# Optimization experiments

Measured on AMD Instinct MI355X. Metric: run time of the kernel, lower is better.

The kernel has to match this reference:

```python
import jax, jax.numpy as jnp
import numpy as np

B = 16384   # batch
S = 6       # fixed number of ABR frequencies
H = 8       # num_heads
HD = 64     # head_dim
D = H * HD  # model width = head_dim * num_heads


def _pe(d):
    # FrequencyPositionalEncoding: pe[i, 0::2] = sin(f_i * div), pe[i, 1::2] = cos(f_i * div)
    freqs = np.array([6.0, 12.0, 18.0, 24.0, 30.0, 0.0], np.float32) / 30.0
    div = np.exp(np.arange(0, d, 2, dtype=np.float32) * (-np.log(10000.0) / d))
    pe = np.zeros((S, d), np.float32)
    pe[:, 0::2] = np.sin(freqs[:, None] * div)
    pe[:, 1::2] = np.cos(freqs[:, None] * div)
    return jnp.asarray(pe)


def _freq_bias():
    # adjacent-frequency bias 0.1, octave pairs (0,1),(1,3) overwritten to 0.05
    b = np.zeros((S, S), np.float32)
    for i in range(S - 1):
        b[i, i + 1] = 0.1
        b[i + 1, i] = 0.1
    for i, j in [(0, 1), (1, 3)]:
        b[i, j] = 0.05
        b[j, i] = 0.05
    return jnp.asarray(b)


def setup_inputs() -> dict:
    key = jax.random.key(0)
    ks = jax.random.split(key, 6)

    def w(k, shape, s=0.05):
        return jax.random.normal(k, shape, jnp.float32) * s

    return {
        "x": jax.random.normal(ks[0], (B, S), jnp.float32),
        "W_in": w(ks[1], (1, D)), "b_in": jnp.zeros((D,), jnp.float32),
        "Wq": w(ks[2], (D, D)), "bq": jnp.zeros((D,), jnp.float32),
        "Wk": w(ks[3], (D, D)), "bk": jnp.zeros((D,), jnp.float32),
        "Wv": w(ks[4], (D, D)), "bv": jnp.zeros((D,), jnp.float32),
        "Wo": w(ks[5], (D, 1)), "bo": jnp.zeros((1,), jnp.float32),
        "gamma": jnp.ones((D,), jnp.float32),
        "beta": jnp.zeros((D,), jnp.float32),
    }


def reference(x, W_in, b_in, Wq, bq, Wk, bk, Wv, bv, Wo, bo, gamma, beta):
    Bn, Sn = x.shape
    Dn = gamma.shape[0]
    hd = Dn // H
    # input projection: scalar token -> D   (Linear(1, D))
    tok = x[..., None] * W_in[0] + b_in                      # (B, S, D)
    tok = tok + _pe(Dn)[None]                                # frequency positional encoding
    # LayerNorm (eps=1e-5)
    mu = tok.mean(-1, keepdims=True)
    var = tok.var(-1, keepdims=True)
    tok = (tok - mu) * jax.lax.rsqrt(var + 1e-5) * gamma + beta
    # q/k/v projections, split heads
    q = (tok @ Wq + bq).reshape(Bn, Sn, H, hd)
    k = (tok @ Wk + bk).reshape(Bn, Sn, H, hd)
    v = (tok @ Wv + bv).reshape(Bn, Sn, H, hd)
    scores = jnp.einsum('bihd,bjhd->bhij', q, k) * (hd ** -0.5)
    scores = scores + _freq_bias()[None, None]               # (B, H, S, S)
    attn = jax.nn.softmax(scores, axis=-1)                   # dropout = identity (eval)
    attended = jnp.einsum('bhij,bjhd->bihd', attn, v).reshape(Bn, Sn, Dn)
    out = (attended @ Wo + bo)[..., 0] + x                   # (B, S) residual
    return out, attn.mean(axis=1)
```

## Files before the change

kernel.cpp:

```cpp
#include <hip/hip_runtime.h>
#include <math.h>

#define WS_STATS 0
#define WS_T     16

__constant__ float FREQ_BIAS[36] = {
    0.0f, 0.05f, 0.0f, 0.0f, 0.0f, 0.0f,
    0.05f, 0.0f, 0.1f, 0.05f, 0.0f, 0.0f,
    0.0f, 0.1f, 0.0f, 0.1f, 0.0f, 0.0f,
    0.0f, 0.05f, 0.1f, 0.0f, 0.1f, 0.0f,
    0.0f, 0.0f, 0.0f, 0.1f, 0.0f, 0.1f,
    0.0f, 0.0f, 0.0f, 0.0f, 0.1f, 0.0f
};

__global__ __launch_bounds__(256) void kA(
    const float* __restrict__ W_in, const float* __restrict__ b_in,
    const float* __restrict__ gamma, const float* __restrict__ beta,
    const float* __restrict__ Wq, const float* __restrict__ bq,
    const float* __restrict__ Wk, const float* __restrict__ bk,
    const float* __restrict__ Wv, const float* __restrict__ bv,
    float* __restrict__ ws, float* __restrict__ part)
{
    __shared__ float ls[8][512];
    __shared__ float partial[4][8][64];
    __shared__ float red[13][4];

    const int tid = threadIdx.x, wave = tid >> 6, lane = tid & 63;
    const int bid = blockIdx.x;
    const int rc = bid & 7, cg = (bid >> 3) & 7, p = bid >> 6;

    const float k_ln = 0.0179889457300305367f;
    const float freqs[6] = {0.2f, 0.4f, 0.6f, 0.8f, 1.0f, 0.0f};
    float wd[2], cc2[2][6], gm[2], bt[2];
    #pragma unroll
    for (int q = 0; q < 2; ++q) {
        const int d = tid + q * 256;
        wd[q] = W_in[d];
        gm[q] = gamma[d];
        bt[q] = beta[d];
        float dv = __expf(-(float)(d & ~1) * k_ln);
        float bi = b_in[d];
        bool odd = (d & 1);
        #pragma unroll
        for (int s = 0; s < 6; ++s) {
            float ph = freqs[s] * dv;
            cc2[q][s] = bi + (odd ? __cosf(ph) : __sinf(ph));
        }
    }
    {
        float sums[7];
        sums[0] = wd[0] + wd[1];
        #pragma unroll
        for (int s = 0; s < 6; ++s) sums[1 + s] = cc2[0][s] + cc2[1][s];
        #pragma unroll
        for (int m = 1; m < 64; m <<= 1) {
            #pragma unroll
            for (int k = 0; k < 7; ++k) sums[k] += __shfl_xor(sums[k], m, 64);
        }
        if (lane == 0) {
            #pragma unroll
            for (int k = 0; k < 7; ++k) red[k][wave] = sums[k];
        }
    }
    __syncthreads();
    const float mw = (red[0][0] + red[0][1] + red[0][2] + red[0][3]) * (1.0f / 512.0f);
    float mc[6];
    #pragma unroll
    for (int s = 0; s < 6; ++s)
        mc[s] = (red[1 + s][0] + red[1 + s][1] + red[1 + s][2] + red[1 + s][3]) * (1.0f / 512.0f);
    __syncthreads();

    float hw[2], hc[2][6];
    #pragma unroll
    for (int q = 0; q < 2; ++q) {
        hw[q] = wd[q] - mw;
        #pragma unroll
        for (int s = 0; s < 6; ++s) hc[q][s] = cc2[q][s] - mc[s];
    }

    if (bid == 0) {
        float moms[13];
        moms[0] = hw[0] * hw[0] + hw[1] * hw[1];
        #pragma unroll
        for (int s = 0; s < 6; ++s) {
            moms[1 + s] = hw[0] * hc[0][s] + hw[1] * hc[1][s];
            moms[7 + s] = hc[0][s] * hc[0][s] + hc[1][s] * hc[1][s];
        }
        #pragma unroll
        for (int m = 1; m < 64; m <<= 1) {
            #pragma unroll
            for (int k = 0; k < 13; ++k) moms[k] += __shfl_xor(moms[k], m, 64);
        }
        if (lane == 0) {
            #pragma unroll
            for (int k = 0; k < 13; ++k) red[k][wave] = moms[k];
        }
    }
    #pragma unroll
    for (int q = 0; q < 2; ++q) {
        const int d = tid + q * 256;
        ls[0][d] = hw[q] * gm[q];
        #pragma unroll
        for (int s = 0; s < 6; ++s) ls[1 + s][d] = hc[q][s] * gm[q];
        ls[7][d] = bt[q];
    }
    __syncthreads();
    if (bid == 0 && tid < 13)
        ws[WS_STATS + tid] = (red[tid][0] + red[tid][1] + red[tid][2] + red[tid][3]) * (1.0f / 512.0f);

    const float* W  = (p == 0) ? Wq : ((p == 1) ? Wk : Wv);
    const float* bb = (p == 0) ? bq : ((p == 1) ? bk : bv);
    const int col = (cg << 6) | lane;
    const int row0 = (rc << 6) | (wave << 4);
    float acc[8] = {0.f, 0.f, 0.f, 0.f, 0.f, 0.f, 0.f, 0.f};
    #pragma unroll
    for (int rr = 0; rr < 16; ++rr) {
        const float wv = W[(row0 + rr) * 512 + col];
        #pragma unroll
        for (int v = 0; v < 8; ++v) acc[v] = fmaf(wv, ls[v][row0 + rr], acc[v]);
    }
    #pragma unroll
    for (int v = 0; v < 8; ++v) partial[wave][v][lane] = acc[v];
    __syncthreads();
    #pragma unroll
    for (int ii = 0; ii < 2; ++ii) {
        const int idx = tid + ii * 256;
        const int v = idx >> 6, cx = idx & 63;
        float t = partial[0][v][cx] + partial[1][v][cx]
                + partial[2][v][cx] + partial[3][v][cx];
        if (v == 7 && rc == 0) t += bb[(cg << 6) | cx];
        part[(size_t)bid * 512 + idx] = t;
    }
}

__global__ __launch_bounds__(256) void kB(const float* __restrict__ part,
                                          const float* __restrict__ Wo,
                                          float* __restrict__ ws)
{
    __shared__ float ab[24][65];
    const int tid = threadIdx.x;
    const int h = blockIdx.x;

    for (int e = tid; e < 24 * 64; e += 256) {
        const int vp = e >> 6, c = e & 63;
        const int p = vp >> 3, v = vp & 7;
        const int stripe = p * 8 + h;
        float t = 0.f;
        #pragma unroll
        for (int rcx = 0; rcx < 8; ++rcx)
            t += part[(size_t)(stripe * 8 + rcx) * 512 + v * 64 + c];
        ab[vp][c] = t;
    }
    __syncthreads();

    if (tid < 64) {
        const int a = tid >> 3, b2 = tid & 7;
        float acc = 0.f;
        #pragma unroll
        for (int c = 0; c < 64; ++c)
            acc = fmaf(ab[a][c], ab[8 + b2][c], acc);
        ws[WS_T + (h << 6) + tid] = acc * 0.125f;
    } else if (tid < 72) {
        const int a = tid - 64;
        float acc = 0.f;
        #pragma unroll
        for (int c = 0; c < 64; ++c)
            acc = fmaf(ab[16 + a][c], Wo[(h << 6) + c], acc);
        ws[WS_T + 512 + (h << 3) + a] = acc;
    }
}

__global__ __launch_bounds__(256) void kC(const float* __restrict__ x,
                                          const float* __restrict__ ws,
                                          const float* __restrict__ bo,
                                          float* __restrict__ out, int total)
{
    __shared__ float T_s[592];
    const int tid = threadIdx.x;
    for (int e = tid; e < 589; e += 256)
        T_s[e] = (e < 576) ? ws[WS_T + e] : ws[WS_STATS + (e - 576)];
    __syncthreads();

    const int g = blockIdx.x * 256 + tid;
    if (g >= total) return;
    const unsigned b = (unsigned)g / 6u;
    const int i = g - (int)b * 6;

    const float* D8 = T_s;
    const float* VD = T_s + 512;
    const float vw = T_s[576];
    const float* cov = T_s + 577;
    const float* vc = T_s + 583;
    const float bo0 = bo[0];

    const float2* xp = (const float2*)(x + (size_t)b * 6u);
    const float2 x01 = xp[0], x23 = xp[1], x45 = xp[2];
    const float al[6] = {x01.x, x01.y, x23.x, x23.y, x45.x, x45.y};

    float r[6], u[6];
    #pragma unroll
    for (int j = 0; j < 6; ++j) {
        float a = al[j];
        float var = fmaf(a, fmaf(a, vw, 2.0f * cov[j]), vc[j]) + 1e-5f;
        r[j] = rsqrtf(var);
        u[j] = a * r[j];
    }

    float bias[6];
    #pragma unroll
    for (int j = 0; j < 6; ++j) bias[j] = FREQ_BIAS[i * 6 + j];

    const float r_i = r[i], u_i = u[i];
    float acc = 0.f;
    float am[6] = {0.f, 0.f, 0.f, 0.f, 0.f, 0.f};

    #pragma unroll
    for (int h = 0; h < 8; ++h) {
        const float* Dh = D8 + h * 64;
        const float* Vh = VD + h * 8;
        const float P1 = Dh[0], P5 = Dh[7], P7 = Dh[56], P9 = Dh[63];
        const float P3i = Dh[(1 + i) * 8], P6i = Dh[(1 + i) * 8 + 7];

        float s[6];
        #pragma unroll
        for (int j = 0; j < 6; ++j) {
            float t1 = fmaf(u[j], P1, fmaf(r[j], Dh[1 + j], P5));
            float t2 = fmaf(u[j], P3i, fmaf(r[j], Dh[(1 + i) * 8 + 1 + j], P6i));
            float t3 = fmaf(u[j], P7, fmaf(r[j], Dh[57 + j], P9));
            s[j] = fmaf(u_i, t1, fmaf(r_i, t2, t3)) + bias[j];
        }
        float m = s[0];
        #pragma unroll
        for (int j = 1; j < 6; ++j) m = fmaxf(m, s[j]);
        float e[6], ssum = 0.f;
        #pragma unroll
        for (int j = 0; j < 6; ++j) { e[j] = __expf(s[j] - m); ssum += e[j]; }
        const float inv = 1.0f / ssum;

        const float av = Vh[0], cvv = Vh[7];
        float ha = 0.f;
        #pragma unroll
        for (int j = 0; j < 6; ++j) {
            float a = e[j] * inv;
            am[j] += a;
            float vp = fmaf(u[j], av, r[j] * Vh[1 + j]);
            ha = fmaf(a, vp, ha);
        }
        acc += ha + cvv;
    }

    out[g] = acc + bo0 + al[i];

    float2* amp = (float2*)(out + total + (size_t)g * 6u);
    amp[0] = make_float2(am[0] * 0.125f, am[1] * 0.125f);
    amp[1] = make_float2(am[2] * 0.125f, am[3] * 0.125f);
    amp[2] = make_float2(am[4] * 0.125f, am[5] * 0.125f);
}

extern "C" void kernel_launch(void* const* d_in, const int* in_sizes, int n_in,
                              void* d_out, int out_size, void* d_ws, size_t ws_size,
                              hipStream_t stream) {
    const float* x     = (const float*)d_in[0];
    const float* W_in  = (const float*)d_in[1];
    const float* b_in  = (const float*)d_in[2];
    const float* Wq    = (const float*)d_in[3];
    const float* bq    = (const float*)d_in[4];
    const float* Wk    = (const float*)d_in[5];
    const float* bk    = (const float*)d_in[6];
    const float* Wv    = (const float*)d_in[7];
    const float* bv    = (const float*)d_in[8];
    const float* Wo    = (const float*)d_in[9];
    const float* bo    = (const float*)d_in[10];
    const float* gamma = (const float*)d_in[11];
    const float* beta  = (const float*)d_in[12];
    float* ws  = (float*)d_ws;
    float* out = (float*)d_out;

    const int total = in_sizes[0];

    kA<<<192, 256, 0, stream>>>(W_in, b_in, gamma, beta, Wq, bq, Wk, bk, Wv, bv, ws, out);
    kB<<<8, 256, 0, stream>>>(out, Wo, ws);
    kC<<<(total + 255) / 256, 256, 0, stream>>>(x, ws, bo, out, total);
}
```

Measured before the change: 20.63 us.

## Split LayerNorm prep into its own kernel and widen projection and output blocks

```diff
diff --git a/kernel.cpp b/kernel.cpp
--- a/kernel.cpp
+++ b/kernel.cpp
@@ -3,6 +3,7 @@
 
 #define WS_STATS 0
 #define WS_T     16
+#define WS_LS    600
 
 __constant__ float FREQ_BIAS[36] = {
     0.0f, 0.05f, 0.0f, 0.0f, 0.0f, 0.0f,
@@ -13,123 +14,137 @@
     0.0f, 0.0f, 0.0f, 0.0f, 0.1f, 0.0f
 };
 
-__global__ __launch_bounds__(256) void kA(
-    const float* __restrict__ W_in, const float* __restrict__ b_in,
-    const float* __restrict__ gamma, const float* __restrict__ beta,
+__global__ __launch_bounds__(512) void kP(const float* __restrict__ W_in,
+                                          const float* __restrict__ b_in,
+                                          const float* __restrict__ gamma,
+                                          const float* __restrict__ beta,
+                                          float* __restrict__ ws)
+{
+    __shared__ float red[13][8];
+    const int d = threadIdx.x, wave = d >> 6, lane = d & 63;
+
+    const float k_ln = 0.0179889457300305367f;
+    const float freqs[6] = {0.2f, 0.4f, 0.6f, 0.8f, 1.0f, 0.0f};
+    const float wd = W_in[d];
+    const float gm = gamma[d];
+    const float bt = beta[d];
+    const float bi = b_in[d];
+    const float dv = __expf(-(float)(d & ~1) * k_ln);
+    const bool odd = (d & 1);
+    float c[6];
+    #pragma unroll
+    for (int s = 0; s < 6; ++s) {
+        float ph = freqs[s] * dv;
+        c[s] = bi + (odd ? __cosf(ph) : __sinf(ph));
+    }
+
+    float sums[7];
+    sums[0] = wd;
+    #pragma unroll
+    for (int s = 0; s < 6; ++s) sums[1 + s] = c[s];
+    #pragma unroll
+    for (int m = 1; m < 64; m <<= 1) {
+        #pragma unroll
+        for (int k = 0; k < 7; ++k) sums[k] += __shfl_xor(sums[k], m, 64);
+    }
+    if (lane == 0) {
+        #pragma unroll
+        for (int k = 0; k < 7; ++k) red[k][wave] = sums[k];
+    }
+    __syncthreads();
+    float mw = 0.f, mc[6] = {0.f, 0.f, 0.f, 0.f, 0.f, 0.f};
+    #pragma unroll
+    for (int j = 0; j < 8; ++j) mw += red[0][j];
+    mw *= (1.0f / 512.0f);
+    #pragma unroll
+    for (int s = 0; s < 6; ++s) {
+        float t = 0.f;
+        #pragma unroll
+        for (int j = 0; j < 8; ++j) t += red[1 + s][j];
+        mc[s] = t * (1.0f / 512.0f);
+    }
+    __syncthreads();
+
+    const float hw = wd - mw;
+    float hc[6];
+    #pragma unroll
+    for (int s = 0; s < 6; ++s) hc[s] = c[s] - mc[s];
+
+    float moms[13];
+    moms[0] = hw * hw;
+    #pragma unroll
+    for (int s = 0; s < 6; ++s) { moms[1 + s] = hw * hc[s]; moms[7 + s] = hc[s] * hc[s]; }
+    #pragma unroll
+    for (int m = 1; m < 64; m <<= 1) {
+        #pragma unroll
+        for (int k = 0; k < 13; ++k) moms[k] += __shfl_xor(moms[k], m, 64);
+    }
+    if (lane == 0) {
+        #pragma unroll
+        for (int k = 0; k < 13; ++k) red[k][wave] = moms[k];
+    }
+    __syncthreads();
+    if (d < 13) {
+        float t = 0.f;
+        #pragma unroll
+        for (int j = 0; j < 8; ++j) t += red[d][j];
+        ws[WS_STATS + d] = t * (1.0f / 512.0f);
+    }
+
+    float4 f0 = make_float4(hw * gm, hc[0] * gm, hc[1] * gm, hc[2] * gm);
+    float4 f1 = make_float4(hc[3] * gm, hc[4] * gm, hc[5] * gm, bt);
+    *(float4*)&ws[WS_LS + d * 8]     = f0;
+    *(float4*)&ws[WS_LS + d * 8 + 4] = f1;
+}
+
+__global__ __launch_bounds__(512) void kA(
     const float* __restrict__ Wq, const float* __restrict__ bq,
     const float* __restrict__ Wk, const float* __restrict__ bk,
     const float* __restrict__ Wv, const float* __restrict__ bv,
-    float* __restrict__ ws, float* __restrict__ part)
-{
-    __shared__ float ls[8][512];
-    __shared__ float partial[4][8][64];
-    __shared__ float red[13][4];
+    const float* __restrict__ ws, float* __restrict__ part)
+{
+    __shared__ float ls_s[64 * 8];
+    __shared__ float partial[8][8][64];
 
     const int tid = threadIdx.x, wave = tid >> 6, lane = tid & 63;
     const int bid = blockIdx.x;
     const int rc = bid & 7, cg = (bid >> 3) & 7, p = bid >> 6;
 
-    const float k_ln = 0.0179889457300305367f;
-    const float freqs[6] = {0.2f, 0.4f, 0.6f, 0.8f, 1.0f, 0.0f};
-    float wd[2], cc2[2][6], gm[2], bt[2];
-    #pragma unroll
-    for (int q = 0; q < 2; ++q) {
-        const int d = tid + q * 256;
-        wd[q] = W_in[d];
-        gm[q] = gamma[d];
-        bt[q] = beta[d];
-        float dv = __expf(-(float)(d & ~1) * k_ln);
-        float bi = b_in[d];
-        bool odd = (d & 1);
-        #pragma unroll
-        for (int s = 0; s < 6; ++s) {
-            float ph = freqs[s] * dv;
-            cc2[q][s] = bi + (odd ? __cosf(ph) : __sinf(ph));
-        }
-    }
-    {
-        float sums[7];
-        sums[0] = wd[0] + wd[1];
-        #pragma unroll
-        for (int s = 0; s < 6; ++s) sums[1 + s] = cc2[0][s] + cc2[1][s];
-        #pragma unroll
-        for (int m = 1; m < 64; m <<= 1) {
-            #pragma unroll
-            for (int k = 0; k < 7; ++k) sums[k] += __shfl_xor(sums[k], m, 64);
-        }
-        if (lane == 0) {
-            #pragma unroll
-            for (int k = 0; k < 7; ++k) red[k][wave] = sums[k];
-        }
-    }
-    __syncthreads();
-    const float mw = (red[0][0] + red[0][1] + red[0][2] + red[0][3]) * (1.0f / 512.0f);
-    float mc[6];
-    #pragma unroll
-    for (int s = 0; s < 6; ++s)
-        mc[s] = (red[1 + s][0] + red[1 + s][1] + red[1 + s][2] + red[1 + s][3]) * (1.0f / 512.0f);
-    __syncthreads();
-
-    float hw[2], hc[2][6];
-    #pragma unroll
-    for (int q = 0; q < 2; ++q) {
-        hw[q] = wd[q] - mw;
-        #pragma unroll
-        for (int s = 0; s < 6; ++s) hc[q][s] = cc2[q][s] - mc[s];
-    }
-
-    if (bid == 0) {
-        float moms[13];
-        moms[0] = hw[0] * hw[0] + hw[1] * hw[1];
-        #pragma unroll
-        for (int s = 0; s < 6; ++s) {
-            moms[1 + s] = hw[0] * hc[0][s] + hw[1] * hc[1][s];
-            moms[7 + s] = hc[0][s] * hc[0][s] + hc[1][s] * hc[1][s];
-        }
-        #pragma unroll
-        for (int m = 1; m < 64; m <<= 1) {
-            #pragma unroll
-            for (int k = 0; k < 13; ++k) moms[k] += __shfl_xor(moms[k], m, 64);
-        }
-        if (lane == 0) {
-            #pragma unroll
-            for (int k = 0; k < 13; ++k) red[k][wave] = moms[k];
-        }
-    }
-    #pragma unroll
-    for (int q = 0; q < 2; ++q) {
-        const int d = tid + q * 256;
-        ls[0][d] = hw[q] * gm[q];
-        #pragma unroll
-        for (int s = 0; s < 6; ++s) ls[1 + s][d] = hc[q][s] * gm[q];
-        ls[7][d] = bt[q];
-    }
-    __syncthreads();
-    if (bid == 0 && tid < 13)
-        ws[WS_STATS + tid] = (red[tid][0] + red[tid][1] + red[tid][2] + red[tid][3]) * (1.0f / 512.0f);
+    ls_s[tid] = ws[WS_LS + rc * 512 + tid];
+    __syncthreads();
 
     const float* W  = (p == 0) ? Wq : ((p == 1) ? Wk : Wv);
     const float* bb = (p == 0) ? bq : ((p == 1) ? bk : bv);
     const int col = (cg << 6) | lane;
-    const int row0 = (rc << 6) | (wave << 4);
+    const int lr0 = wave << 3;
+    const int row0 = (rc << 6) | lr0;
+
     float acc[8] = {0.f, 0.f, 0.f, 0.f, 0.f, 0.f, 0.f, 0.f};
     #pragma unroll
-    for (int rr = 0; rr < 16; ++rr) {
+    for (int rr = 0; rr < 8; ++rr) {
         const float wv = W[(row0 + rr) * 512 + col];
-        #pragma unroll
-        for (int v = 0; v < 8; ++v) acc[v] = fmaf(wv, ls[v][row0 + rr], acc[v]);
+        const float4 f0 = *(const float4*)&ls_s[(lr0 + rr) * 8];
+        const float4 f1 = *(const float4*)&ls_s[(lr0 + rr) * 8 + 4];
+        acc[0] = fmaf(wv, f0.x, acc[0]);
+        acc[1] = fmaf(wv, f0.y, acc[1]);
+        acc[2] = fmaf(wv, f0.z, acc[2]);
+        acc[3] = fmaf(wv, f0.w, acc[3]);
+        acc[4] = fmaf(wv, f1.x, acc[4]);
+        acc[5] = fmaf(wv, f1.y, acc[5]);
+        acc[6] = fmaf(wv, f1.z, acc[6]);
+        acc[7] = fmaf(wv, f1.w, acc[7]);
     }
     #pragma unroll
     for (int v = 0; v < 8; ++v) partial[wave][v][lane] = acc[v];
     __syncthreads();
-    #pragma unroll
-    for (int ii = 0; ii < 2; ++ii) {
-        const int idx = tid + ii * 256;
-        const int v = idx >> 6, cx = idx & 63;
-        float t = partial[0][v][cx] + partial[1][v][cx]
-                + partial[2][v][cx] + partial[3][v][cx];
+
+    {
+        const int v = tid >> 6, cx = tid & 63;
+        float t = 0.f;
+        #pragma unroll
+        for (int w = 0; w < 8; ++w) t += partial[w][v][cx];
         if (v == 7 && rc == 0) t += bb[(cg << 6) | cx];
-        part[(size_t)bid * 512 + idx] = t;
+        part[(size_t)bid * 512 + tid] = t;
     }
 }
 
@@ -170,18 +185,18 @@
     }
 }
 
-__global__ __launch_bounds__(256) void kC(const float* __restrict__ x,
+__global__ __launch_bounds__(384) void kC(const float* __restrict__ x,
                                           const float* __restrict__ ws,
                                           const float* __restrict__ bo,
                                           float* __restrict__ out, int total)
 {
     __shared__ float T_s[592];
     const int tid = threadIdx.x;
-    for (int e = tid; e < 589; e += 256)
+    for (int e = tid; e < 589; e += 384)
         T_s[e] = (e < 576) ? ws[WS_T + e] : ws[WS_STATS + (e - 576)];
     __syncthreads();
 
-    const int g = blockIdx.x * 256 + tid;
+    const int g = blockIdx.x * 384 + tid;
     if (g >= total) return;
     const unsigned b = (unsigned)g / 6u;
     const int i = g - (int)b * 6;
@@ -205,7 +220,6 @@
         r[j] = rsqrtf(var);
         u[j] = a * r[j];
     }
-
     float bias[6];
     #pragma unroll
     for (int j = 0; j < 6; ++j) bias[j] = FREQ_BIAS[i * 6 + j];
@@ -250,7 +264,6 @@
     }
 
     out[g] = acc + bo0 + al[i];
-
     float2* amp = (float2*)(out + total + (size_t)g * 6u);
     amp[0] = make_float2(am[0] * 0.125f, am[1] * 0.125f);
     amp[1] = make_float2(am[2] * 0.125f, am[3] * 0.125f);
@@ -278,7 +291,8 @@
 
     const int total = in_sizes[0];
 
-    kA<<<192, 256, 0, stream>>>(W_in, b_in, gamma, beta, Wq, bq, Wk, bk, Wv, bv, ws, out);
+    kP<<<1, 512, 0, stream>>>(W_in, b_in, gamma, beta, ws);
+    kA<<<192, 512, 0, stream>>>(Wq, bq, Wk, bk, Wv, bv, ws, out);
     kB<<<8, 256, 0, stream>>>(out, Wo, ws);
-    kC<<<(total + 255) / 256, 256, 0, stream>>>(x, ws, bo, out, total);
-}
+    kC<<<256, 384, 0, stream>>>(x, ws, bo, out, total);
+}
```

After: 22.90 us. 11.0% more time.
